# Performance work log

Measured on AMD Instinct MI355X. Metric: run time of the kernel, lower is better.

## Reference

```python
import jax, jax.numpy as jnp
import numpy as np
import math

B, L, D, H = 4, 2048, 1024, 16
DH = D // H


def setup_inputs() -> dict:
    key = jax.random.key(0)
    ks = jax.random.split(key, 12)
    s = 0.02
    q = jax.random.normal(ks[0], (B, L, D), jnp.float32)
    k = jax.random.normal(ks[1], (B, L, D), jnp.float32)
    v = jax.random.normal(ks[2], (B, L, D), jnp.float32)
    # realistic padding: each sequence has a valid prefix of length in [L//2, L]
    lengths = jax.random.randint(ks[3], (B,), L // 2, L + 1)
    attention_mask = jnp.arange(L)[None, :] < lengths[:, None]  # [B, L] bool
    Wq = jax.random.normal(ks[4], (D, D), jnp.float32) * s
    bq = jnp.zeros((D,), jnp.float32)
    Wk = jax.random.normal(ks[5], (D, D), jnp.float32) * s
    bk = jnp.zeros((D,), jnp.float32)
    Wv = jax.random.normal(ks[6], (D, D), jnp.float32) * s
    bv = jnp.zeros((D,), jnp.float32)
    Wc = jax.random.normal(ks[7], (D, D), jnp.float32) * s
    bc = jnp.zeros((D,), jnp.float32)
    return {"q": q, "k": k, "v": v, "attention_mask": attention_mask,
            "Wq": Wq, "bq": bq, "Wk": Wk, "bk": bk,
            "Wv": Wv, "bv": bv, "Wc": Wc, "bc": bc}


def reference(q, k, v, attention_mask, Wq, bq, Wk, bk, Wv, bv, Wc, bc):
    b, l, d = q.shape
    # projections -> [B, H, L, DH]
    wq = (q @ Wq.T + bq).reshape(b, l, H, DH).transpose(0, 2, 1, 3)
    wk = (k @ Wk.T + bk).reshape(b, l, H, DH).transpose(0, 2, 1, 3)
    wv = (v @ Wv.T + bv).reshape(b, l, H, DH).transpose(0, 2, 1, 3)
    scores = jnp.einsum('bhqd,bhkd->bhqk', wq, wk) / math.sqrt(DH)  # [B,H,L,L]
    # fused causal + padding mask (additive, finfo.min like the torch code)
    pad2d = attention_mask[:, :, None] & attention_mask[:, None, :]  # [B,L,L]
    causal = jnp.tril(jnp.ones((l, l), dtype=bool))
    mask = pad2d[:, None, :, :] & causal[None, None, :, :]  # [B,1,L,L] -> broadcast over heads
    min_val = jnp.finfo(scores.dtype).min
    scores = scores + jnp.where(mask, jnp.float32(0.0), min_val).astype(scores.dtype)
    att = jax.nn.softmax(scores, axis=-1)
    out = jnp.einsum('bhqk,bhkd->bhqd', att, wv)  # [B,H,L,DH]
    out = out.transpose(0, 2, 1, 3).reshape(b, l, H * DH)
    return out @ Wc.T + bc
```

## Files before the change

### kernel.cpp

```cpp
#include <hip/hip_runtime.h>
#include <stdint.h>

typedef __bf16 bf16x8 __attribute__((ext_vector_type(8)));
typedef float f32x4 __attribute__((ext_vector_type(4)));
typedef unsigned short ushort8 __attribute__((ext_vector_type(8)));
typedef unsigned short ushort4v __attribute__((ext_vector_type(4)));

constexpr int CB = 4;
constexpr int CL = 2048;
constexpr int CD = 1024;
constexpr int CH = 16;
constexpr int CDH = 64;
constexpr int CM = CB * CL;

__device__ __forceinline__ unsigned short f2bf(float f) {
  union { float f; unsigned u; } x; x.f = f;
  unsigned r = x.u + 0x7fffu + ((x.u >> 16) & 1u);
  return (unsigned short)(r >> 16);
}
__device__ __forceinline__ float bf2f(unsigned short b) {
  union { unsigned u; float f; } x; x.u = ((unsigned)b) << 16;
  return x.f;
}

__device__ __forceinline__ void gld_lds16(const void* g, void* l) {
  __builtin_amdgcn_global_load_lds((const __attribute__((address_space(1))) void*)g,
                                   (__attribute__((address_space(3))) void*)l, 16, 0, 0);
}

#define MFMA16(a, b, c) __builtin_amdgcn_mfma_f32_16x16x32_bf16((a), (b), (c), 0, 0, 0)


__global__ __launch_bounds__(256) void cvt_all(const float* __restrict__ q,
                                               const float* __restrict__ k,
                                               const float* __restrict__ v,
                                               const float* __restrict__ Wq,
                                               const float* __restrict__ Wk,
                                               const float* __restrict__ Wv,
                                               const float* __restrict__ Wc,
                                               unsigned short* __restrict__ oq,
                                               unsigned short* __restrict__ ok,
                                               unsigned short* __restrict__ ov,
                                               unsigned short* __restrict__ oWq,
                                               unsigned short* __restrict__ oWk,
                                               unsigned short* __restrict__ oWv,
                                               unsigned short* __restrict__ oWc) {
  int bi = blockIdx.x;
  const float* s;
  unsigned short* d;
  int i;
  if (bi < 2048) {
    const int w = bi >> 9;
    i = (bi & 511) * 256 + threadIdx.x;
    s = w == 0 ? Wq : w == 1 ? Wk : w == 2 ? Wv : Wc;
    d = w == 0 ? oWq : w == 1 ? oWk : w == 2 ? oWv : oWc;
  } else {
    bi -= 2048;
    const int w = bi >> 12;
    i = (bi & 4095) * 256 + threadIdx.x;
    s = w == 0 ? q : w == 1 ? k : v;
    d = w == 0 ? oq : w == 1 ? ok : ov;
  }
  const float4* sp = (const float4*)s;
  float4 a = sp[2 * i], b = sp[2 * i + 1];
  ushort8 o;
  o[0] = f2bf(a.x); o[1] = f2bf(a.y); o[2] = f2bf(a.z); o[3] = f2bf(a.w);
  o[4] = f2bf(b.x); o[5] = f2bf(b.y); o[6] = f2bf(b.z); o[7] = f2bf(b.w);
  ((ushort8*)d)[i] = o;
}


__global__ __launch_bounds__(256) void lens_kernel(const int* __restrict__ mask,
                                                   int* __restrict__ lens) {
  __shared__ int part[4];
  const int b = blockIdx.x;
  int cnt = 0;
  for (int i = threadIdx.x; i < CL; i += 256) cnt += (mask[b * CL + i] != 0) ? 1 : 0;
#pragma unroll
  for (int off = 32; off; off >>= 1) cnt += __shfl_down(cnt, off);
  if ((threadIdx.x & 63) == 0) part[threadIdx.x >> 6] = cnt;
  __syncthreads();
  if (threadIdx.x == 0) lens[b] = part[0] + part[1] + part[2] + part[3];
}


#define GEMM_WAIT2(kt, nkt)                                             \
  {                                                                     \
    if ((kt) + 1 < (nkt))                                               \
      asm volatile("s_waitcnt vmcnt(2)" ::: "memory");                  \
    else                                                                \
      asm volatile("s_waitcnt vmcnt(0)" ::: "memory");                  \
    __builtin_amdgcn_s_barrier();                                       \
    asm volatile("" ::: "memory");                                      \
  }


__global__ __launch_bounds__(512) void gemm_qkv(const unsigned short* __restrict__ Xq,
                                                const unsigned short* __restrict__ Xk,
                                                const unsigned short* __restrict__ Xv,
                                                const unsigned short* __restrict__ Wb,
                                                const float* __restrict__ bq,
                                                const float* __restrict__ bk,
                                                const float* __restrict__ bv,
                                                unsigned short* __restrict__ Qp,
                                                unsigned short* __restrict__ Kp,
                                                unsigned short* __restrict__ Vt,
                                                float qscale) {
  __shared__ unsigned short Asm[3][128 * 32];
  __shared__ unsigned short Bsm[3][128 * 32];
  const int tid = threadIdx.x;
  const int w = tid >> 6, ln = tid & 63, lr = ln & 15, lq = ln >> 4;
  const int nbx = 24;
  const int cpx = (int)gridDim.x >> 3;
  const int bid = ((int)blockIdx.x & 7) * cpx + ((int)blockIdx.x >> 3);
  const int bm = (bid / nbx) << 7;
  const int bnG = (bid % nbx) << 7;
  const int which = bnG >> 10, bn = bnG & 1023;
  const unsigned short* A = which == 0 ? Xq : which == 1 ? Xk : Xv;
  const unsigned short* Bw = Wb + ((size_t)which << 20);
  const float* bias = which == 0 ? bq : which == 1 ? bk : bv;
  const float alpha = which == 0 ? qscale : 1.0f;
  const int wr = (w >> 1) << 5, wc = (w & 1) << 6;

  f32x4 acc[2][4] = {};
  const int arow = tid >> 2, akc = (tid & 3) << 3;

  auto stage = [&](int buf, int k0) {
    gld_lds16(A + (size_t)(bm + arow) * CD + k0 + akc, (void*)(Asm[buf] + w * 512));
    gld_lds16(Bw + (size_t)(bn + arow) * CD + k0 + akc, (void*)(Bsm[buf] + w * 512));
  };

  stage(0, 0);
  stage(1, 32);

  const int nkt = CD >> 5;
  int cur = 0;
  for (int kt = 0; kt < nkt; ++kt) {
    GEMM_WAIT2(kt, nkt);
    if (kt + 2 < nkt) {
      int nb = cur + 2;
      if (nb >= 3) nb -= 3;
      stage(nb, (kt + 2) << 5);
    }
    bf16x8 af[2], bfr[4];
#pragma unroll
    for (int f = 0; f < 2; ++f)
      af[f] = *(const bf16x8*)(Asm[cur] + ((wr + f * 16 + lr) * 32 + lq * 8));
#pragma unroll
    for (int f = 0; f < 4; ++f)
      bfr[f] = *(const bf16x8*)(Bsm[cur] + ((wc + f * 16 + lr) * 32 + lq * 8));
#pragma unroll
    for (int fm = 0; fm < 2; ++fm)
#pragma unroll
      for (int fn = 0; fn < 4; ++fn)
        acc[fm][fn] = MFMA16(af[fm], bfr[fn], acc[fm][fn]);
    if (++cur == 3) cur = 0;
  }

#pragma unroll
  for (int fm = 0; fm < 2; ++fm) {
    const int row0 = bm + wr + fm * 16 + lq * 4;
#pragma unroll
    for (int fn = 0; fn < 4; ++fn) {
      const int col = bn + wc + fn * 16 + lr;
      const float bb = bias[col];
      if (which == 2) {
        const int b = row0 >> 11, lrow = row0 & (CL - 1);
        const int hh = col >> 6, dh = col & 63;
        ushort4v pk;
#pragma unroll
        for (int j = 0; j < 4; ++j) pk[j] = f2bf(acc[fm][fn][j] + bb);
        *(ushort4v*)(Vt + (((size_t)((b * CH + hh) * CDH + dh)) << 11) + lrow) = pk;
      } else {
        unsigned short* outp = which == 0 ? Qp : Kp;
#pragma unroll
        for (int j = 0; j < 4; ++j)
          outp[(size_t)(row0 + j) * CD + col] = f2bf((acc[fm][fn][j] + bb) * alpha);
      }
    }
  }
}


__global__ __launch_bounds__(512) void gemm_out(const unsigned short* __restrict__ A,
                                                const unsigned short* __restrict__ Bw,
                                                const float* __restrict__ bias,
                                                float* __restrict__ Cout) {
  __shared__ unsigned short Asm[3][128 * 32];
  __shared__ unsigned short Bsm[3][128 * 32];
  const int tid = threadIdx.x;
  const int w = tid >> 6, ln = tid & 63, lr = ln & 15, lq = ln >> 4;
  const int nbx = CD >> 7;
  const int cpx = (int)gridDim.x >> 3;
  const int bid = ((int)blockIdx.x & 7) * cpx + ((int)blockIdx.x >> 3);
  const int bm = (bid / nbx) << 7;
  const int bn = (bid % nbx) << 7;
  const int wr = (w >> 1) << 5, wc = (w & 1) << 6;

  f32x4 acc[2][4] = {};
  const int arow = tid >> 2, akc = (tid & 3) << 3;

  auto stage = [&](int buf, int k0) {
    gld_lds16(A + (size_t)(bm + arow) * CD + k0 + akc, (void*)(Asm[buf] + w * 512));
    gld_lds16(Bw + (size_t)(bn + arow) * CD + k0 + akc, (void*)(Bsm[buf] + w * 512));
  };

  stage(0, 0);
  stage(1, 32);

  const int nkt = CD >> 5;
  int cur = 0;
  for (int kt = 0; kt < nkt; ++kt) {
    GEMM_WAIT2(kt, nkt);
    if (kt + 2 < nkt) {
      int nb = cur + 2;
      if (nb >= 3) nb -= 3;
      stage(nb, (kt + 2) << 5);
    }
    bf16x8 af[2], bfr[4];
#pragma unroll
    for (int f = 0; f < 2; ++f)
      af[f] = *(const bf16x8*)(Asm[cur] + ((wr + f * 16 + lr) * 32 + lq * 8));
#pragma unroll
    for (int f = 0; f < 4; ++f)
      bfr[f] = *(const bf16x8*)(Bsm[cur] + ((wc + f * 16 + lr) * 32 + lq * 8));
#pragma unroll
    for (int fm = 0; fm < 2; ++fm)
#pragma unroll
      for (int fn = 0; fn < 4; ++fn)
        acc[fm][fn] = MFMA16(af[fm], bfr[fn], acc[fm][fn]);
    if (++cur == 3) cur = 0;
  }

#pragma unroll
  for (int fm = 0; fm < 2; ++fm) {
    const int row0 = bm + wr + fm * 16 + lq * 4;
#pragma unroll
    for (int fn = 0; fn < 4; ++fn) {
      const int col = bn + wc + fn * 16 + lr;
      const float bb = bias[col];
#pragma unroll
      for (int j = 0; j < 4; ++j)
        Cout[(size_t)(row0 + j) * CD + col] = acc[fm][fn][j] + bb;
    }
  }
}


__global__ __launch_bounds__(256) void meanv_kernel(const unsigned short* __restrict__ Vt,
                                                    float* __restrict__ meanv) {
  const int row = blockIdx.x * 4 + (threadIdx.x >> 6);
  const int ln = threadIdx.x & 63;
  const ushort8* p = (const ushort8*)(Vt + (size_t)row * CL);
  float s = 0.f;
#pragma unroll
  for (int it = 0; it < 4; ++it) {
    ushort8 v = p[it * 64 + ln];
#pragma unroll
    for (int j = 0; j < 8; ++j) s += bf2f(v[j]);
  }
#pragma unroll
  for (int off = 32; off; off >>= 1) s += __shfl_down(s, off);
  if (ln == 0) meanv[row] = s * (1.f / (float)CL);
}


#define LOADK(kt, dst)                                                              \
  {                                                                                 \
    const int kb_ = (kt) << 6;                                                      \
    for (int cf_ = 0; cf_ < 4; ++cf_)                                               \
      for (int hf_ = 0; hf_ < 2; ++hf_)                                             \
        dst[cf_][hf_] = *(const bf16x8*)(Kbase + (size_t)(kb_ + cf_ * 16 + lr) * CD + \
                                         hf_ * 32 + lq * 8);                        \
  }

#define VLOAD_FB(kt, dst)                                                           \
  {                                                                                 \
    const int kb_ = (kt) << 6;                                                      \
    for (int df_ = 0; df_ < 4; ++df_)                                               \
      for (int hf_ = 0; hf_ < 2; ++hf_)                                             \
        dst[df_][hf_] = *(const bf16x8*)(Vbase + (((size_t)(df_ * 16 + lr)) << 11) +  \
                                         kb_ + hf_ * 32 + lq * 8);                  \
  }


__global__ __launch_bounds__(64, 2) void attn_w64(const unsigned short* __restrict__ Qp,
                                                  const unsigned short* __restrict__ Kp,
                                                  const unsigned short* __restrict__ Vt,
                                                  const int* __restrict__ lens,
                                                  unsigned short* __restrict__ attno) {
  __shared__ unsigned short Ps[64][72];
  const int i = blockIdx.x;
  const int xcd = i & 7, bh8 = (i >> 3) & 7, slot = i >> 6;
  const int qc = 31 - slot;
  const int bh = bh8 * 8 + xcd;
  const int b = bh >> 4, h = bh & 15;
  const int rowbase = qc << 6;
  const int len = lens[b];
  if (rowbase >= len) return;

  const int tid = threadIdx.x, lr = tid & 15, lq = tid >> 4;

  const unsigned short* Kbase = Kp + (size_t)(b * CL) * CD + h * 64;
  const unsigned short* Vbase = Vt + ((size_t)(bh * 64) << 11);
  const unsigned short* Qbase = Qp + (size_t)(b * CL + rowbase) * CD + h * 64;

  bf16x8 qa[4][2];
#pragma unroll
  for (int rs = 0; rs < 4; ++rs)
#pragma unroll
    for (int hf = 0; hf < 2; ++hf)
      qa[rs][hf] = *(const bf16x8*)(Qbase + (size_t)(rs * 16 + lr) * CD + hf * 32 + lq * 8);

  f32x4 o[4][4] = {};
  float lsum[4][4] = {};
  const int kdiag = qc;

  bf16x8 kf[4][2], vb[4][2];

  for (int kt = 0; kt <= kdiag; ++kt) {
    const bool dm = (kt == kdiag);
    const int kb = kt << 6;
    LOADK(kt, kf);
    VLOAD_FB(kt, vb);
    __builtin_amdgcn_sched_barrier(0);

#pragma unroll
    for (int rs = 0; rs < 4; ++rs) {
      f32x4 s_[4];
#pragma unroll
      for (int cf = 0; cf < 4; ++cf) {
        f32x4 z = {};
        z = MFMA16(qa[rs][0], kf[cf][0], z);
        z = MFMA16(qa[rs][1], kf[cf][1], z);
        s_[cf] = z;
      }
#pragma unroll
      for (int cf = 0; cf < 4; ++cf) {
#pragma unroll
        for (int j = 0; j < 4; ++j) {
          float p = __builtin_amdgcn_exp2f(s_[cf][j]);
          if (dm) {
            const int key = kb + cf * 16 + lr;
            const int row = rowbase + rs * 16 + lq * 4 + j;
            p = (key > row) ? 0.f : p;
          }
          lsum[rs][j] += p;
          Ps[rs * 16 + lq * 4 + j][cf * 16 + lr] =
              (unsigned short)(__builtin_bit_cast(unsigned int, p) >> 16);
        }
      }
    }

    bf16x8 pa[4][2];
#pragma unroll
    for (int rs = 0; rs < 4; ++rs)
#pragma unroll
      for (int hf = 0; hf < 2; ++hf)
        pa[rs][hf] = *(const bf16x8*)(&Ps[rs * 16 + lr][hf * 32 + lq * 8]);

#pragma unroll
    for (int df = 0; df < 4; ++df) {
#pragma unroll
      for (int rs = 0; rs < 4; ++rs) {
        o[rs][df] = MFMA16(pa[rs][0], vb[df][0], o[rs][df]);
        o[rs][df] = MFMA16(pa[rs][1], vb[df][1], o[rs][df]);
      }
    }
  }

  float inv[4][4];
#pragma unroll
  for (int rs = 0; rs < 4; ++rs)
#pragma unroll
    for (int j = 0; j < 4; ++j) {
      float t = lsum[rs][j];
      t += __shfl_xor(t, 1);
      t += __shfl_xor(t, 2);
      t += __shfl_xor(t, 4);
      t += __shfl_xor(t, 8);
      inv[rs][j] = __builtin_amdgcn_rcpf(t);
    }

#pragma unroll
  for (int rs = 0; rs < 4; ++rs)
#pragma unroll
    for (int df = 0; df < 4; ++df)
#pragma unroll
      for (int j = 0; j < 4; ++j)
        attno[(size_t)(b * CL + rowbase + rs * 16 + lq * 4 + j) * CD + h * 64 + df * 16 +
              lr] = f2bf(o[rs][df][j] * inv[rs][j]);
}


#define TILE_FB(kt, KF, KN)                                                         \
  {                                                                                 \
    const bool dm_ = (kt) == kdiag;                                                 \
    const int kb_ = (kt) << 6;                                                      \
    f32x4 s_[2][4];                                                                 \
    for (int rs_ = 0; rs_ < 2; ++rs_)                                               \
      for (int cf_ = 0; cf_ < 4; ++cf_) {                                           \
        f32x4 z_ = {};                                                              \
        z_ = MFMA16(qa[rs_][0], KF[cf_][0], z_);                                    \
        z_ = MFMA16(qa[rs_][1], KF[cf_][1], z_);                                    \
        s_[rs_][cf_] = z_;                                                          \
      }                                                                             \
    VLOAD_FB(kt, vb);                                                               \
    if ((kt) < kdiag) LOADK((kt) + 1, KN);                                          \
    __builtin_amdgcn_sched_barrier(0);                                              \
    for (int rs_ = 0; rs_ < 2; ++rs_)                                               \
      for (int cf_ = 0; cf_ < 4; ++cf_)                                             \
        for (int j_ = 0; j_ < 4; ++j_) {                                            \
          float p_ = __builtin_amdgcn_exp2f(s_[rs_][cf_][j_]);                      \
          if (dm_) {                                                                \
            const int key_ = kb_ + cf_ * 16 + lr;                                   \
            const int row_ = rowbase + rs_ * 16 + lq * 4 + j_;                      \
            p_ = (key_ > row_) ? 0.f : p_;                                          \
          }                                                                         \
          lsum[rs_][j_] += p_;                                                      \
          Ps[rs_ * 16 + lq * 4 + j_][cf_ * 16 + lr] =                               \
              (unsigned short)(__builtin_bit_cast(unsigned int, p_) >> 16);         \
        }                                                                           \
    bf16x8 pa_[2][2];                                                               \
    for (int rs_ = 0; rs_ < 2; ++rs_)                                               \
      for (int hf_ = 0; hf_ < 2; ++hf_)                                             \
        pa_[rs_][hf_] = *(const bf16x8*)(&Ps[rs_ * 16 + lr][hf_ * 32 + lq * 8]);    \
    for (int df_ = 0; df_ < 4; ++df_) {                                             \
      o[0][df_] = MFMA16(pa_[0][0], vb[df_][0], o[0][df_]);                         \
      o[0][df_] = MFMA16(pa_[0][1], vb[df_][1], o[0][df_]);                         \
      o[1][df_] = MFMA16(pa_[1][0], vb[df_][0], o[1][df_]);                         \
      o[1][df_] = MFMA16(pa_[1][1], vb[df_][1], o[1][df_]);                         \
    }                                                                               \
  }

__global__ __launch_bounds__(64, 2) void attn_fb(const unsigned short* __restrict__ Qp,
                                                 const unsigned short* __restrict__ Kp,
                                                 const unsigned short* __restrict__ Vt,
                                                 const int* __restrict__ lens,
                                                 unsigned short* __restrict__ attno) {
  __shared__ unsigned short Ps[32][72];
  const int i = blockIdx.x;
  const int xcd = i & 7, bh8 = (i >> 3) & 7, slot = i >> 6;
  const int qt = 15 - (slot >> 2), wv = slot & 3;
  const int bh = bh8 * 8 + xcd;
  const int b = bh >> 4, h = bh & 15;
  const int rowbase = (qt << 7) + (wv << 5);
  const int len = lens[b];
  if (rowbase >= len) return;

  const int tid = threadIdx.x, lr = tid & 15, lq = tid >> 4;

  const unsigned short* Kbase = Kp + (size_t)(b * CL) * CD + h * 64;
  const unsigned short* Vbase = Vt + ((size_t)(bh * 64) << 11);
  const unsigned short* Qbase = Qp + (size_t)(b * CL + rowbase) * CD + h * 64;

  bf16x8 qa[2][2];
#pragma unroll
  for (int rs = 0; rs < 2; ++rs)
#pragma unroll
    for (int hf = 0; hf < 2; ++hf)
      qa[rs][hf] = *(const bf16x8*)(Qbase + (size_t)(rs * 16 + lr) * CD + hf * 32 + lq * 8);

  f32x4 o[2][4] = {};
  float lsum[2][4] = {};
  const int kdiag = rowbase >> 6;

  bf16x8 kfA[4][2], kfB[4][2], vb[4][2];
  LOADK(0, kfA);

  int kt = 0;
  while (true) {
    TILE_FB(kt, kfA, kfB);
    if (kt == kdiag) break;
    ++kt;
    TILE_FB(kt, kfB, kfA);
    if (kt == kdiag) break;
    ++kt;
  }

  float inv[2][4];
#pragma unroll
  for (int rs = 0; rs < 2; ++rs)
#pragma unroll
    for (int j = 0; j < 4; ++j) {
      float t = lsum[rs][j];
      t += __shfl_xor(t, 1);
      t += __shfl_xor(t, 2);
      t += __shfl_xor(t, 4);
      t += __shfl_xor(t, 8);
      inv[rs][j] = __builtin_amdgcn_rcpf(t);
    }

#pragma unroll
  for (int rs = 0; rs < 2; ++rs)
#pragma unroll
    for (int df = 0; df < 4; ++df)
#pragma unroll
      for (int j = 0; j < 4; ++j)
        attno[(size_t)(b * CL + rowbase + rs * 16 + lq * 4 + j) * CD + h * 64 + df * 16 +
              lr] = f2bf(o[rs][df][j] * inv[rs][j]);
}


__global__ __launch_bounds__(256) void padfix_kernel(const int* __restrict__ lens,
                                                     const float* __restrict__ meanv,
                                                     unsigned short* __restrict__ attno) {
  const int q = blockIdx.x & (CL - 1);
  const int b = blockIdx.x >> 11;
  if (q < lens[b]) return;
#pragma unroll
  for (int i = 0; i < 4; ++i) {
    const int col = threadIdx.x + i * 256;
    attno[(size_t)(b * CL + q) * CD + col] = f2bf(meanv[b * CD + col]);
  }
}


extern "C" void kernel_launch(void* const* d_in, const int* in_sizes, int n_in,
                              void* d_out, int out_size, void* d_ws, size_t ws_size,
                              hipStream_t stream) {
  const float* q  = (const float*)d_in[0];
  const float* k  = (const float*)d_in[1];
  const float* v  = (const float*)d_in[2];
  const int*   am = (const int*)d_in[3];
  const float* Wq = (const float*)d_in[4];
  const float* bq = (const float*)d_in[5];
  const float* Wk = (const float*)d_in[6];
  const float* bk = (const float*)d_in[7];
  const float* Wv = (const float*)d_in[8];
  const float* bv = (const float*)d_in[9];
  const float* Wc = (const float*)d_in[10];
  const float* bc = (const float*)d_in[11];
  float* out = (float*)d_out;

  unsigned short* Wqb = (unsigned short*)d_ws;
  unsigned short* Wkb = Wqb + (1 << 20);
  unsigned short* Wvb = Wkb + (1 << 20);
  unsigned short* Wcb = Wvb + (1 << 20);
  unsigned short* Xq  = Wcb + (1 << 20);
  unsigned short* Xk  = Xq + (size_t)CM * CD;
  unsigned short* Xv  = Xk + (size_t)CM * CD;
  unsigned short* Qp  = Xv + (size_t)CM * CD;
  unsigned short* Kp  = Qp + (size_t)CM * CD;
  unsigned short* Vt  = Kp + (size_t)CM * CD;
  float* meanv = (float*)(Vt + (size_t)CM * CD);
  int* lens = (int*)(meanv + CB * CD);
  unsigned short* X = Xq;

  lens_kernel<<<CB, 256, 0, stream>>>(am, lens);
  cvt_all<<<14336, 256, 0, stream>>>(q, k, v, Wq, Wk, Wv, Wc, Xq, Xk, Xv,
                                     Wqb, Wkb, Wvb, Wcb);

  const float QSCALE = 0.125f * 1.44269504f;

  gemm_qkv<<<1536, 512, 0, stream>>>(Xq, Xk, Xv, Wqb, bq, bk, bv, Qp, Kp, Vt, QSCALE);

  meanv_kernel<<<1024, 256, 0, stream>>>(Vt, meanv);

  hipFuncAttributes fa{};
  bool w64_ok = false;
  if (hipFuncGetAttributes(&fa, (const void*)attn_w64) == hipSuccess)
    w64_ok = (fa.localSizeBytes == 0);
  if (w64_ok)
    attn_w64<<<2048, 64, 0, stream>>>(Qp, Kp, Vt, lens, X);
  else
    attn_fb<<<4096, 64, 0, stream>>>(Qp, Kp, Vt, lens, X);

  padfix_kernel<<<CB * CL, 256, 0, stream>>>(lens, meanv, X);

  gemm_out<<<512, 512, 0, stream>>>(X, Wcb, bc, out);
}
```

Before: 226.8 us.

## Share K/V tiles across four waves via triple-buffered LDS staging

```diff
diff --git a/kernel.cpp b/kernel.cpp
--- a/kernel.cpp
+++ b/kernel.cpp
@@ -265,6 +265,158 @@
 }
 
 
+__global__ __launch_bounds__(256, 2) void attn_blk(const unsigned short* __restrict__ Qp,
+                                                   const unsigned short* __restrict__ Kp,
+                                                   const unsigned short* __restrict__ Vt,
+                                                   const int* __restrict__ lens,
+                                                   unsigned short* __restrict__ attno) {
+  __shared__ unsigned short Ks[3][64 * 64];
+  __shared__ unsigned short Vs[3][64 * 64];
+  __shared__ unsigned short Ps[4][32][72];
+  const int i = blockIdx.x;
+  const int xcd = i & 7, bh8 = (i >> 3) & 7, slot = i >> 6;
+  const int qt = 15 - slot;
+  const int bh = bh8 * 8 + xcd;
+  const int b = bh >> 4, h = bh & 15;
+  const int qbase = qt << 7;
+  const int len = lens[b];
+  if (qbase >= len) return;
+
+  const int tid = threadIdx.x, w = tid >> 6, ln = tid & 63, lr = ln & 15, lq = ln >> 4;
+  const int rowbase = qbase + (w << 5);
+  const int kdw = rowbase >> 6;
+  const int ntiles = 2 * qt + 2;
+
+  const unsigned short* Kbase = Kp + (size_t)(b * CL) * CD + h * 64;
+  const unsigned short* Vbase = Vt + ((size_t)(bh * 64) << 11);
+  const unsigned short* Qbase = Qp + (size_t)(b * CL + rowbase) * CD + h * 64;
+
+  const int srow = (w << 4) + (ln >> 3);
+  const int scol = (ln & 7) << 3;
+  auto stage = [&](int buf, int kt) {
+    const int kb = kt << 6;
+#pragma unroll
+    for (int p = 0; p < 2; ++p) {
+      gld_lds16(Kbase + (size_t)(kb + srow + p * 8) * CD + scol,
+                (void*)(Ks[buf] + (w << 10) + (p << 9)));
+      gld_lds16(Vbase + (size_t)(srow + p * 8) * CL + kb + scol,
+                (void*)(Vs[buf] + (w << 10) + (p << 9)));
+    }
+  };
+
+  bf16x8 qa[2][2];
+#pragma unroll
+  for (int rs = 0; rs < 2; ++rs)
+#pragma unroll
+    for (int hf = 0; hf < 2; ++hf)
+      qa[rs][hf] = *(const bf16x8*)(Qbase + (size_t)(rs * 16 + lr) * CD + hf * 32 + lq * 8);
+  __builtin_amdgcn_sched_barrier(0);
+  stage(0, 0);
+  __builtin_amdgcn_sched_barrier(0);
+  stage(1, 1);
+  __builtin_amdgcn_sched_barrier(0);
+
+  f32x4 o[2][4] = {};
+  float lsum[2][4] = {};
+
+  int cur = 0;
+  for (int kt = 0; kt < ntiles; ++kt) {
+    if (kt + 1 < ntiles)
+      asm volatile("s_waitcnt vmcnt(4)" ::: "memory");
+    else
+      asm volatile("s_waitcnt vmcnt(0)" ::: "memory");
+    __builtin_amdgcn_s_barrier();
+    asm volatile("" ::: "memory");
+    if (kt + 2 < ntiles) {
+      int nb = cur + 2;
+      if (nb >= 3) nb -= 3;
+      stage(nb, kt + 2);
+    }
+
+    if (kt <= kdw) {
+      const bool dm = (kt == kdw);
+      const int kb = kt << 6;
+      const unsigned short* Kc = Ks[cur];
+      const unsigned short* Vc = Vs[cur];
+
+      bf16x8 kf[4][2];
+#pragma unroll
+      for (int cf = 0; cf < 4; ++cf)
+#pragma unroll
+        for (int hf = 0; hf < 2; ++hf)
+          kf[cf][hf] = *(const bf16x8*)(Kc + (cf * 16 + lr) * 64 + hf * 32 + lq * 8);
+
+#pragma unroll
+      for (int rs = 0; rs < 2; ++rs) {
+        f32x4 s_[4];
+#pragma unroll
+        for (int cf = 0; cf < 4; ++cf) {
+          f32x4 z = {};
+          z = MFMA16(qa[rs][0], kf[cf][0], z);
+          z = MFMA16(qa[rs][1], kf[cf][1], z);
+          s_[cf] = z;
+        }
+#pragma unroll
+        for (int cf = 0; cf < 4; ++cf) {
+#pragma unroll
+          for (int j = 0; j < 4; ++j) {
+            float p = __builtin_amdgcn_exp2f(s_[cf][j]);
+            if (dm) {
+              const int key = kb + cf * 16 + lr;
+              const int row = rowbase + rs * 16 + lq * 4 + j;
+              p = (key > row) ? 0.f : p;
+            }
+            lsum[rs][j] += p;
+            Ps[w][rs * 16 + lq * 4 + j][cf * 16 + lr] =
+                (unsigned short)(__builtin_bit_cast(unsigned int, p) >> 16);
+          }
+        }
+      }
+
+      bf16x8 pa[2][2];
+#pragma unroll
+      for (int rs = 0; rs < 2; ++rs)
+#pragma unroll
+        for (int hf = 0; hf < 2; ++hf)
+          pa[rs][hf] = *(const bf16x8*)(&Ps[w][rs * 16 + lr][hf * 32 + lq * 8]);
+
+#pragma unroll
+      for (int df = 0; df < 4; ++df) {
+        const bf16x8 vb0 = *(const bf16x8*)(Vc + (df * 16 + lr) * 64 + lq * 8);
+        const bf16x8 vb1 = *(const bf16x8*)(Vc + (df * 16 + lr) * 64 + 32 + lq * 8);
+        o[0][df] = MFMA16(pa[0][0], vb0, o[0][df]);
+        o[0][df] = MFMA16(pa[0][1], vb1, o[0][df]);
+        o[1][df] = MFMA16(pa[1][0], vb0, o[1][df]);
+        o[1][df] = MFMA16(pa[1][1], vb1, o[1][df]);
+      }
+    }
+    if (++cur == 3) cur = 0;
+  }
+
+  float inv[2][4];
+#pragma unroll
+  for (int rs = 0; rs < 2; ++rs)
+#pragma unroll
+    for (int j = 0; j < 4; ++j) {
+      float t = lsum[rs][j];
+      t += __shfl_xor(t, 1);
+      t += __shfl_xor(t, 2);
+      t += __shfl_xor(t, 4);
+      t += __shfl_xor(t, 8);
+      inv[rs][j] = __builtin_amdgcn_rcpf(t);
+    }
+
+#pragma unroll
+  for (int rs = 0; rs < 2; ++rs)
+#pragma unroll
+    for (int df = 0; df < 4; ++df)
+#pragma unroll
+      for (int j = 0; j < 4; ++j)
+        attno[(size_t)(b * CL + rowbase + rs * 16 + lq * 4 + j) * CD + h * 64 + df * 16 +
+              lr] = f2bf(o[rs][df][j] * inv[rs][j]);
+}
+
+
 #define LOADK(kt, dst)                                                              \
   {                                                                                 \
     const int kb_ = (kt) << 6;                                                      \
@@ -282,116 +434,6 @@
         dst[df_][hf_] = *(const bf16x8*)(Vbase + (((size_t)(df_ * 16 + lr)) << 11) +  \
                                          kb_ + hf_ * 32 + lq * 8);                  \
   }
-
-
-__global__ __launch_bounds__(64, 2) void attn_w64(const unsigned short* __restrict__ Qp,
-                                                  const unsigned short* __restrict__ Kp,
-                                                  const unsigned short* __restrict__ Vt,
-                                                  const int* __restrict__ lens,
-                                                  unsigned short* __restrict__ attno) {
-  __shared__ unsigned short Ps[64][72];
-  const int i = blockIdx.x;
-  const int xcd = i & 7, bh8 = (i >> 3) & 7, slot = i >> 6;
-  const int qc = 31 - slot;
-  const int bh = bh8 * 8 + xcd;
-  const int b = bh >> 4, h = bh & 15;
-  const int rowbase = qc << 6;
-  const int len = lens[b];
-  if (rowbase >= len) return;
-
-  const int tid = threadIdx.x, lr = tid & 15, lq = tid >> 4;
-
-  const unsigned short* Kbase = Kp + (size_t)(b * CL) * CD + h * 64;
-  const unsigned short* Vbase = Vt + ((size_t)(bh * 64) << 11);
-  const unsigned short* Qbase = Qp + (size_t)(b * CL + rowbase) * CD + h * 64;
-
-  bf16x8 qa[4][2];
-#pragma unroll
-  for (int rs = 0; rs < 4; ++rs)
-#pragma unroll
-    for (int hf = 0; hf < 2; ++hf)
-      qa[rs][hf] = *(const bf16x8*)(Qbase + (size_t)(rs * 16 + lr) * CD + hf * 32 + lq * 8);
-
-  f32x4 o[4][4] = {};
-  float lsum[4][4] = {};
-  const int kdiag = qc;
-
-  bf16x8 kf[4][2], vb[4][2];
-
-  for (int kt = 0; kt <= kdiag; ++kt) {
-    const bool dm = (kt == kdiag);
-    const int kb = kt << 6;
-    LOADK(kt, kf);
-    VLOAD_FB(kt, vb);
-    __builtin_amdgcn_sched_barrier(0);
-
-#pragma unroll
-    for (int rs = 0; rs < 4; ++rs) {
-      f32x4 s_[4];
-#pragma unroll
-      for (int cf = 0; cf < 4; ++cf) {
-        f32x4 z = {};
-        z = MFMA16(qa[rs][0], kf[cf][0], z);
-        z = MFMA16(qa[rs][1], kf[cf][1], z);
-        s_[cf] = z;
-      }
-#pragma unroll
-      for (int cf = 0; cf < 4; ++cf) {
-#pragma unroll
-        for (int j = 0; j < 4; ++j) {
-          float p = __builtin_amdgcn_exp2f(s_[cf][j]);
-          if (dm) {
-            const int key = kb + cf * 16 + lr;
-            const int row = rowbase + rs * 16 + lq * 4 + j;
-            p = (key > row) ? 0.f : p;
-          }
-          lsum[rs][j] += p;
-          Ps[rs * 16 + lq * 4 + j][cf * 16 + lr] =
-              (unsigned short)(__builtin_bit_cast(unsigned int, p) >> 16);
-        }
-      }
-    }
-
-    bf16x8 pa[4][2];
-#pragma unroll
-    for (int rs = 0; rs < 4; ++rs)
-#pragma unroll
-      for (int hf = 0; hf < 2; ++hf)
-        pa[rs][hf] = *(const bf16x8*)(&Ps[rs * 16 + lr][hf * 32 + lq * 8]);
-
-#pragma unroll
-    for (int df = 0; df < 4; ++df) {
-#pragma unroll
-      for (int rs = 0; rs < 4; ++rs) {
-        o[rs][df] = MFMA16(pa[rs][0], vb[df][0], o[rs][df]);
-        o[rs][df] = MFMA16(pa[rs][1], vb[df][1], o[rs][df]);
-      }
-    }
-  }
-
-  float inv[4][4];
-#pragma unroll
-  for (int rs = 0; rs < 4; ++rs)
-#pragma unroll
-    for (int j = 0; j < 4; ++j) {
-      float t = lsum[rs][j];
-      t += __shfl_xor(t, 1);
-      t += __shfl_xor(t, 2);
-      t += __shfl_xor(t, 4);
-      t += __shfl_xor(t, 8);
-      inv[rs][j] = __builtin_amdgcn_rcpf(t);
-    }
-
-#pragma unroll
-  for (int rs = 0; rs < 4; ++rs)
-#pragma unroll
-    for (int df = 0; df < 4; ++df)
-#pragma unroll
-      for (int j = 0; j < 4; ++j)
-        attno[(size_t)(b * CL + rowbase + rs * 16 + lq * 4 + j) * CD + h * 64 + df * 16 +
-              lr] = f2bf(o[rs][df][j] * inv[rs][j]);
-}
-
 
 #define TILE_FB(kt, KF, KN)                                                         \
   {                                                                                 \
@@ -558,11 +600,11 @@
   meanv_kernel<<<1024, 256, 0, stream>>>(Vt, meanv);
 
   hipFuncAttributes fa{};
-  bool w64_ok = false;
-  if (hipFuncGetAttributes(&fa, (const void*)attn_w64) == hipSuccess)
-    w64_ok = (fa.localSizeBytes == 0);
-  if (w64_ok)
-    attn_w64<<<2048, 64, 0, stream>>>(Qp, Kp, Vt, lens, X);
+  bool blk_ok = false;
+  if (hipFuncGetAttributes(&fa, (const void*)attn_blk) == hipSuccess)
+    blk_ok = (fa.localSizeBytes == 0);
+  if (blk_ok)
+    attn_blk<<<1024, 256, 0, stream>>>(Qp, Kp, Vt, lens, X);
   else
     attn_fb<<<4096, 64, 0, stream>>>(Qp, Kp, Vt, lens, X);
 
```

After: 194.1 us. 1.17x faster.
